# Kernel optimization log

Hardware: AMD Instinct MI355X
Metric: run time of the kernel (lower is better)

Reference implementation:

```python
import jax, jax.numpy as jnp
import numpy as np

N, E, G = 50000, 500000, 64
DIN, ED, H1, H2, HD, OUT = 128, 32, 256, 128, 64, 8


def setup_inputs() -> dict:
    key = jax.random.key(0)
    ks = jax.random.split(key, 20)
    g = lambda i, shape: (jax.random.normal(ks[i], shape, jnp.float32) * 0.05)
    return dict(
        node_attr=jax.random.normal(ks[0], (N, DIN), jnp.float32),
        edge_attr=jax.random.normal(ks[1], (E, ED), jnp.float32),
        edge_src=jax.random.randint(ks[2], (E,), 0, N, jnp.int32),
        edge_dst=jax.random.randint(ks[3], (E,), 0, N, jnp.int32),
        batch=jnp.sort(jax.random.randint(ks[4], (N,), 0, G, jnp.int32)),
        Wl1=g(5, (DIN, H1)), bl1=jnp.zeros((H1,), jnp.float32),
        Wr1=g(6, (DIN, H1)), br1=jnp.zeros((H1,), jnp.float32),
        We1=g(7, (ED, H1)), att1=g(8, (H1,)), b1=jnp.zeros((H1,), jnp.float32),
        Wl2=g(9, (H1, H2)), bl2=jnp.zeros((H2,), jnp.float32),
        Wr2=g(10, (H1, H2)), br2=jnp.zeros((H2,), jnp.float32),
        We2=g(11, (ED, H2)), att2=g(12, (H2,)), b2=jnp.zeros((H2,), jnp.float32),
        Wd1=g(13, (H2, HD)), bd1=jnp.zeros((HD,), jnp.float32),
        bn_gamma=jnp.ones((HD,), jnp.float32), bn_beta=jnp.zeros((HD,), jnp.float32),
        bn_mean=jnp.zeros((HD,), jnp.float32), bn_var=jnp.ones((HD,), jnp.float32),
        Wd2=g(14, (HD, OUT)), bd2=jnp.zeros((OUT,), jnp.float32),
    )


def gatv2(x, src, dst, eattr, Wl, bl, Wr, br, We, att, bias, n):
    # PyG GATv2Conv, heads=1: add self-loops (fill_value='mean' for edge_attr)
    ones = jnp.ones((eattr.shape[0],), x.dtype)
    deg = jax.ops.segment_sum(ones, dst, n)
    loop_attr = jax.ops.segment_sum(eattr, dst, n) / jnp.maximum(deg, 1.0)[:, None]
    loop = jnp.arange(n, dtype=src.dtype)
    src_ = jnp.concatenate([src, loop])
    dst_ = jnp.concatenate([dst, loop])
    eattr_ = jnp.concatenate([eattr, loop_attr], axis=0)
    xl = x @ Wl + bl  # [n, C] source transform (lin_l)
    xr = x @ Wr + br  # [n, C] dest transform (lin_r)
    # edge-wise GATv2 score: a^T LeakyReLU(xl_j + xr_i + We e_ij)
    e = jax.nn.leaky_relu(xl[src_] + xr[dst_] + eattr_ @ We, 0.2) @ att  # [E+n]
    m = jax.ops.segment_max(e, dst_, n)
    w = jnp.exp(e - m[dst_])
    denom = jax.ops.segment_sum(w, dst_, n)
    alpha = w / denom[dst_]
    return jax.ops.segment_sum(alpha[:, None] * xl[src_], dst_, n) + bias


def reference(node_attr, edge_attr, edge_src, edge_dst, batch,
              Wl1, bl1, Wr1, br1, We1, att1, b1,
              Wl2, bl2, Wr2, br2, We2, att2, b2,
              Wd1, bd1, bn_gamma, bn_beta, bn_mean, bn_var, Wd2, bd2):
    x = jax.nn.relu(gatv2(node_attr, edge_src, edge_dst, edge_attr,
                          Wl1, bl1, Wr1, br1, We1, att1, b1, N))
    x = jax.nn.relu(gatv2(x, edge_src, edge_dst, edge_attr,
                          Wl2, bl2, Wr2, br2, We2, att2, b2, N))
    # global mean pool over graphs
    cnt = jax.ops.segment_sum(jnp.ones((N,), x.dtype), batch, G)
    x = jax.ops.segment_sum(x, batch, G) / jnp.maximum(cnt, 1.0)[:, None]
    x = x @ Wd1 + bd1
    # BatchNorm1d in eval mode (running stats); dropout is identity in eval
    x = (x - bn_mean) / jnp.sqrt(bn_var + 1e-5) * bn_gamma + bn_beta
    x = jax.nn.leaky_relu(x, 0.1)
    return x @ Wd2 + bd2
```

## Files before the change

### kernel.cpp

```cpp
#include <hip/hip_runtime.h>
#include <cstdint>
#include <cstddef>
#include <cmath>

constexpr int Nn = 50000;
constexpr int Ne = 500000;
constexpr int Gg = 64;
constexpr int DIN = 128, ED = 32, H1 = 256, H2 = 128, HD = 64, NOUT = 8;

typedef __attribute__((ext_vector_type(8))) short bf16x8;
typedef __attribute__((ext_vector_type(4))) float f32x4;

__device__ __forceinline__ unsigned short f2bf(float x) {
    unsigned u = __float_as_uint(x);
    u += 0x7FFFu + ((u >> 16) & 1u);
    return (unsigned short)(u >> 16);
}
__device__ __forceinline__ float bf2f(unsigned short h) {
    return __uint_as_float(((unsigned)h) << 16);
}

__global__ void count_deg_kernel(const int* __restrict__ dst, int* __restrict__ deg) {
    int e = blockIdx.x * 256 + threadIdx.x;
    if (e < Ne) atomicAdd(&deg[dst[e]], 1);
}

__global__ __launch_bounds__(1024) void scan_kernel(const int* __restrict__ deg,
                                                    int* __restrict__ row_start) {
    __shared__ int part[1024];
    int t = threadIdx.x;
    const int chunk = (Nn + 1023) / 1024;
    int lo = t * chunk;
    int hi = min(lo + chunk, Nn);
    int s = 0;
    for (int i = lo; i < hi; i++) s += deg[i];
    part[t] = s;
    __syncthreads();
    for (int off = 1; off < 1024; off <<= 1) {
        int add = (t >= off) ? part[t - off] : 0;
        __syncthreads();
        part[t] += add;
        __syncthreads();
    }
    int base = (t == 0) ? 0 : part[t - 1];
    for (int i = lo; i < hi; i++) { row_start[i] = base; base += deg[i]; }
    if (t == 0) row_start[Nn] = Ne;
}

__global__ void scatter_kernel(const int* __restrict__ dst, const int* __restrict__ row_start,
                               int* __restrict__ cursor, int* __restrict__ perm) {
    int e = blockIdx.x * 256 + threadIdx.x;
    if (e < Ne) {
        int d = dst[e];
        int p = atomicAdd(&cursor[d], 1);
        perm[row_start[d] + p] = e;
    }
}

__global__ void build_sd_kernel(const int* __restrict__ perm, const int* __restrict__ src,
                                const int* __restrict__ dst,
                                int* __restrict__ srcv, int* __restrict__ dstv) {
    int j = blockIdx.x * 256 + threadIdx.x;
    if (j < Ne) {
        int e = perm[j];
        srcv[j] = src[e];
        dstv[j] = dst[e];
    }
}

__global__ void loop_attr_kernel(const int* __restrict__ row_start, const int* __restrict__ perm,
                                 const float* __restrict__ eattr, float* __restrict__ loop_attr) {
    int tid = blockIdx.x * 256 + threadIdx.x;
    if (tid >= Nn * 8) return;
    int i = tid >> 3, q = (tid & 7) << 2;
    int r0 = row_start[i], r1 = row_start[i + 1];
    float4 s = make_float4(0.f, 0.f, 0.f, 0.f);
    for (int j = r0; j < r1; j++) {
        int e = perm[j];
        float4 v = *(const float4*)(eattr + (size_t)e * ED + q);
        s.x += v.x; s.y += v.y; s.z += v.z; s.w += v.w;
    }
    float inv = 1.0f / fmaxf((float)(r1 - r0), 1.0f);
    *(float4*)(loop_attr + (size_t)i * ED + q) =
        make_float4(s.x * inv, s.y * inv, s.z * inv, s.w * inv);
}

__global__ void cvt_split_kernel(const float* __restrict__ src,
                                 unsigned short* __restrict__ hi,
                                 unsigned short* __restrict__ lo, int n4) {
    int idx = blockIdx.x * 256 + threadIdx.x;
    if (idx >= n4) return;
    float4 v = *(const float4*)(src + (size_t)idx * 4);
    float x[4] = {v.x, v.y, v.z, v.w};
    unsigned short h[4], l[4];
#pragma unroll
    for (int c = 0; c < 4; c++) {
        h[c] = f2bf(x[c]);
        l[c] = f2bf(x[c] - bf2f(h[c]));
    }
    *(ushort4*)(hi + (size_t)idx * 4) = make_ushort4(h[0], h[1], h[2], h[3]);
    *(ushort4*)(lo + (size_t)idx * 4) = make_ushort4(l[0], l[1], l[2], l[3]);
}

__global__ void cvt_W_kernel(const float* __restrict__ We,
                             unsigned short* __restrict__ whi,
                             unsigned short* __restrict__ wlo, int C) {
    int t = blockIdx.x * 256 + threadIdx.x;
    if (t >= C * ED) return;
    int c = t >> 5, k = t & 31;
    float x = We[(size_t)k * C + c];
    unsigned short h = f2bf(x);
    whi[t] = h;
    wlo[t] = f2bf(x - bf2f(h));
}

__global__ __launch_bounds__(256) void gemm_bias2_kernel(const float* __restrict__ A,
                                                         const float* __restrict__ W0,
                                                         const float* __restrict__ bias0,
                                                         float* __restrict__ C0,
                                                         const float* __restrict__ W1,
                                                         const float* __restrict__ bias1,
                                                         float* __restrict__ C1,
                                                         int M, int K, int Ncols) {
    const float* W = blockIdx.z ? W1 : W0;
    const float* bias = blockIdx.z ? bias1 : bias0;
    float* C = blockIdx.z ? C1 : C0;
    __shared__ float As[16][68];
    __shared__ float Bs[16][68];
    const int m0 = blockIdx.y * 64, n0 = blockIdx.x * 64;
    const int tid = threadIdx.x;
    const int tx = tid & 15, ty = tid >> 4;
    float acc[4][4] = {};
    const int ar = tid >> 2, ac4 = (tid & 3) << 2;
    const int br = tid >> 4, bc4 = (tid & 15) << 2;
    const bool arow_ok = (m0 + ar < M);

    float4 av = make_float4(0.f, 0.f, 0.f, 0.f);
    if (arow_ok) av = *(const float4*)(A + (size_t)(m0 + ar) * K + ac4);
    float4 bv = *(const float4*)(W + (size_t)br * Ncols + n0 + bc4);

    for (int k0 = 0; k0 < K; k0 += 16) {
        As[ac4 + 0][ar] = av.x; As[ac4 + 1][ar] = av.y;
        As[ac4 + 2][ar] = av.z; As[ac4 + 3][ar] = av.w;
        *(float4*)&Bs[br][bc4] = bv;
        __syncthreads();
        if (k0 + 16 < K) {
            if (arow_ok) av = *(const float4*)(A + (size_t)(m0 + ar) * K + k0 + 16 + ac4);
            bv = *(const float4*)(W + (size_t)(k0 + 16 + br) * Ncols + n0 + bc4);
        }
#pragma unroll
        for (int k = 0; k < 16; k++) {
            float a[4], b[4];
#pragma unroll
            for (int i = 0; i < 4; i++) a[i] = As[k][ty * 4 + i];
#pragma unroll
            for (int j = 0; j < 4; j++) b[j] = Bs[k][tx * 4 + j];
#pragma unroll
            for (int i = 0; i < 4; i++)
#pragma unroll
                for (int j = 0; j < 4; j++) acc[i][j] = fmaf(a[i], b[j], acc[i][j]);
        }
        __syncthreads();
    }
#pragma unroll
    for (int i = 0; i < 4; i++) {
        int m = m0 + ty * 4 + i;
        if (m < M) {
            float4 o;
            o.x = acc[i][0] + bias[n0 + tx * 4 + 0];
            o.y = acc[i][1] + bias[n0 + tx * 4 + 1];
            o.z = acc[i][2] + bias[n0 + tx * 4 + 2];
            o.w = acc[i][3] + bias[n0 + tx * 4 + 3];
            *(float4*)(C + (size_t)m * Ncols + n0 + tx * 4) = o;
        }
    }
}

template <int C>
__global__ __launch_bounds__((C / 64) * 64) void score_mfma3_kernel(
    int count, const int* __restrict__ perm,
    const int* __restrict__ srcv, const int* __restrict__ dstv,
    const unsigned short* __restrict__ ehi, const unsigned short* __restrict__ elo,
    const float* __restrict__ xl, const float* __restrict__ xr,
    const unsigned short* __restrict__ wthi, const unsigned short* __restrict__ wtlo,
    const float* __restrict__ att, float* __restrict__ sc_out) {
    constexpr int WPB = C / 64;
    constexpr int NTHR = WPB * 64;
    __shared__ unsigned short Ah[64 * 40], Al[64 * 40];
    __shared__ float pw[WPB][64];
    const int tid = threadIdx.x;
    const int j0 = blockIdx.x * 64;

    for (int t = tid; t < 64 * 4; t += NTHR) {
        int row = t >> 2, part = t & 3;
        int j = min(j0 + row, count - 1);
        int e = perm ? perm[j] : j;
        *(uint4*)&Ah[row * 40 + part * 8] = *(const uint4*)(ehi + (size_t)e * ED + part * 8);
        *(uint4*)&Al[row * 40 + part * 8] = *(const uint4*)(elo + (size_t)e * ED + part * 8);
    }
    __syncthreads();

    const int wv = tid >> 6, lane = tid & 63;
    const int g = lane >> 4, li = lane & 15;
    const int cb = wv * 64 + g * 4;

    bf16x8 af_h[4], af_l[4];
#pragma unroll
    for (int m = 0; m < 4; m++) {
        int col = wv * 64 + m * 16 + li;
        af_h[m] = *(const bf16x8*)(wthi + (size_t)col * ED + g * 8);
        af_l[m] = *(const bf16x8*)(wtlo + (size_t)col * ED + g * 8);
    }
    float4 attv[4];
#pragma unroll
    for (int m = 0; m < 4; m++) attv[m] = *(const float4*)(att + cb + m * 16);

    int s0, d0, s1, d1, s2, d2, s3, d3;
    {
        int j;
        j = min(j0 + 0 * 16 + li, count - 1); s0 = srcv ? srcv[j] : j; d0 = dstv ? dstv[j] : j;
        j = min(j0 + 1 * 16 + li, count - 1); s1 = srcv ? srcv[j] : j; d1 = dstv ? dstv[j] : j;
        j = min(j0 + 2 * 16 + li, count - 1); s2 = srcv ? srcv[j] : j; d2 = dstv ? dstv[j] : j;
        j = min(j0 + 3 * 16 + li, count - 1); s3 = srcv ? srcv[j] : j; d3 = dstv ? dstv[j] : j;
    }

    auto pf = [&](int n, int sE, int dE, bf16x8& bh, bf16x8& bl,
                  float4 (&xlv)[4], float4 (&xrv)[4]) {
        bh = *(const bf16x8*)&Ah[(n * 16 + li) * 40 + g * 8];
        bl = *(const bf16x8*)&Al[(n * 16 + li) * 40 + g * 8];
        const float* pl = xl + (size_t)sE * C + cb;
        const float* pr = xr + (size_t)dE * C + cb;
#pragma unroll
        for (int m = 0; m < 4; m++) {
            xlv[m] = *(const float4*)(pl + m * 16);
            xrv[m] = *(const float4*)(pr + m * 16);
        }
    };
    auto comp = [&](int n, bf16x8 bh, bf16x8 bl,
                    const float4 (&xlv)[4], const float4 (&xrv)[4]) {
        f32x4 acc[4];
#pragma unroll
        for (int m = 0; m < 4; m++) {
            acc[m][0] = xlv[m].x + xrv[m].x; acc[m][1] = xlv[m].y + xrv[m].y;
            acc[m][2] = xlv[m].z + xrv[m].z; acc[m][3] = xlv[m].w + xrv[m].w;
        }
#pragma unroll
        for (int m = 0; m < 4; m++) {
            acc[m] = __builtin_amdgcn_mfma_f32_16x16x32_bf16(af_h[m], bh, acc[m], 0, 0, 0);
            acc[m] = __builtin_amdgcn_mfma_f32_16x16x32_bf16(af_h[m], bl, acc[m], 0, 0, 0);
            acc[m] = __builtin_amdgcn_mfma_f32_16x16x32_bf16(af_l[m], bh, acc[m], 0, 0, 0);
        }
        float s = 0.f;
#pragma unroll
        for (int m = 0; m < 4; m++) {
            const float av[4] = {attv[m].x, attv[m].y, attv[m].z, attv[m].w};
#pragma unroll
            for (int r = 0; r < 4; r++) {
                float z = acc[m][r];
                z = z > 0.f ? z : 0.2f * z;
                s = fmaf(z, av[r], s);
            }
        }
        s += __shfl_xor(s, 16);
        s += __shfl_xor(s, 32);
        if (lane < 16) pw[wv][n * 16 + li] = s;
    };

    bf16x8 bhA, blA, bhB, blB;
    float4 xlA[4], xrA[4], xlB[4], xrB[4];
    pf(0, s0, d0, bhA, blA, xlA, xrA);
    pf(1, s1, d1, bhB, blB, xlB, xrB);
    comp(0, bhA, blA, xlA, xrA);
    pf(2, s2, d2, bhA, blA, xlA, xrA);
    comp(1, bhB, blB, xlB, xrB);
    pf(3, s3, d3, bhB, blB, xlB, xrB);
    comp(2, bhA, blA, xlA, xrA);
    comp(3, bhB, blB, xlB, xrB);

    __syncthreads();
    if (tid < 64) {
        float s = pw[0][tid];
#pragma unroll
        for (int w = 1; w < WPB; w++) s += pw[w][tid];
        int j = j0 + tid;
        if (j < count) sc_out[j] = s;
    }
}

template <int C>
__global__ __launch_bounds__(256) void aggregate2_kernel(
    const int* __restrict__ row_start, const int* __restrict__ srcv,
    const float* __restrict__ scores, const float* __restrict__ sscore,
    const float* __restrict__ xl, const float* __restrict__ bias,
    float* __restrict__ xout) {
    constexpr int VP = C / 64;
    const int wave = threadIdx.x >> 6, lane = threadIdx.x & 63;
    const int i = blockIdx.x * 4 + wave;
    if (i >= Nn) return;
    const int r0 = row_start[i], r1 = row_start[i + 1];

    float mx = sscore[i];
    for (int j = r0 + lane; j < r1; j += 64) mx = fmaxf(mx, scores[j]);
#pragma unroll
    for (int off = 32; off >= 1; off >>= 1) mx = fmaxf(mx, __shfl_xor(mx, off));

    float l = 0.f;
    float acc[VP];
#pragma unroll
    for (int j = 0; j < VP; j++) acc[j] = 0.f;

    float wA[4], xA[4][VP];
    auto load_batch = [&](int j0, float* w, float (*x)[VP]) {
#pragma unroll
        for (int q = 0; q < 4; q++) {
            int j = min(j0 + q, r1 - 1);
            w[q] = scores[j];
            const float* p = xl + (size_t)srcv[j] * C + lane * VP;
            if constexpr (VP == 4) {
                float4 v = *(const float4*)p;
                x[q][0] = v.x; x[q][1] = v.y; x[q][2] = v.z; x[q][3] = v.w;
            } else {
                float2 v = *(const float2*)p;
                x[q][0] = v.x; x[q][1] = v.y;
            }
        }
    };
    if (r0 < r1) load_batch(r0, wA, xA);

    for (int j0 = r0; j0 < r1; j0 += 4) {
        float wB[4], xB[4][VP];
        if (j0 + 4 < r1) load_batch(j0 + 4, wB, xB);
        const int nb = min(4, r1 - j0);
        for (int q = 0; q < nb; q++) {
            float w = __expf(wA[q] - mx);
            l += w;
#pragma unroll
            for (int j = 0; j < VP; j++) acc[j] = fmaf(w, xA[q][j], acc[j]);
        }
        if (j0 + 4 < r1) {
#pragma unroll
            for (int q = 0; q < 4; q++) {
                wA[q] = wB[q];
#pragma unroll
                for (int j = 0; j < VP; j++) xA[q][j] = xB[q][j];
            }
        }
    }

    {
        float w = __expf(sscore[i] - mx);
        l += w;
        const float* p = xl + (size_t)i * C + lane * VP;
        if constexpr (VP == 4) {
            float4 v = *(const float4*)p;
            acc[0] = fmaf(w, v.x, acc[0]); acc[1] = fmaf(w, v.y, acc[1]);
            acc[2] = fmaf(w, v.z, acc[2]); acc[3] = fmaf(w, v.w, acc[3]);
        } else {
            float2 v = *(const float2*)p;
            acc[0] = fmaf(w, v.x, acc[0]); acc[1] = fmaf(w, v.y, acc[1]);
        }
    }

    float invl = 1.0f / l;
    float* xo = xout + (size_t)i * C + lane * VP;
    if constexpr (VP == 4) {
        float4 bv = *(const float4*)(bias + lane * 4);
        float4 o;
        o.x = fmaxf(fmaf(acc[0], invl, bv.x), 0.f);
        o.y = fmaxf(fmaf(acc[1], invl, bv.y), 0.f);
        o.z = fmaxf(fmaf(acc[2], invl, bv.z), 0.f);
        o.w = fmaxf(fmaf(acc[3], invl, bv.w), 0.f);
        *(float4*)xo = o;
    } else {
        float2 bv = *(const float2*)(bias + lane * 2);
        float2 o;
        o.x = fmaxf(fmaf(acc[0], invl, bv.x), 0.f);
        o.y = fmaxf(fmaf(acc[1], invl, bv.y), 0.f);
        *(float2*)xo = o;
    }
}

__global__ __launch_bounds__(128) void pool2_kernel(const float* __restrict__ x2,
                                                    const int* __restrict__ batch,
                                                    float* __restrict__ pooled,
                                                    float* __restrict__ cnt) {
    const int c = threadIdx.x;
    const int chunk = (Nn + gridDim.x - 1) / gridDim.x;
    int lo = blockIdx.x * chunk;
    int hi = min(lo + chunk, Nn);
    if (lo >= hi) return;
    int gcur = batch[lo];
    float acc = 0.f, ncnt = 0.f;
    for (int i = lo; i < hi; i++) {
        int g = batch[i];
        if (g != gcur) {
            atomicAdd(&pooled[gcur * H2 + c], acc);
            if (c == 0) atomicAdd(&cnt[gcur], ncnt);
            acc = 0.f; ncnt = 0.f; gcur = g;
        }
        acc += x2[(size_t)i * H2 + c];
        ncnt += 1.f;
    }
    atomicAdd(&pooled[gcur * H2 + c], acc);
    if (c == 0) atomicAdd(&cnt[gcur], ncnt);
}

__global__ __launch_bounds__(64) void head_kernel(
    const float* __restrict__ pooled, const float* __restrict__ cnt,
    const float* __restrict__ Wd1, const float* __restrict__ bd1,
    const float* __restrict__ gamma, const float* __restrict__ beta,
    const float* __restrict__ mean, const float* __restrict__ var,
    const float* __restrict__ Wd2, const float* __restrict__ bd2,
    float* __restrict__ out) {
    __shared__ float xm[H2];
    __shared__ float h[HD];
    int g = blockIdx.x, t = threadIdx.x;
    float c = fmaxf(cnt[g], 1.0f);
    for (int i = t; i < H2; i += 64) xm[i] = pooled[g * H2 + i] / c;
    __syncthreads();
    float a = bd1[t];
    for (int k = 0; k < H2; k++) a = fmaf(xm[k], Wd1[k * HD + t], a);
    a = (a - mean[t]) / sqrtf(var[t] + 1e-5f) * gamma[t] + beta[t];
    a = a > 0.f ? a : 0.1f * a;
    h[t] = a;
    __syncthreads();
    if (t < NOUT) {
        float o = bd2[t];
        for (int k = 0; k < HD; k++) o = fmaf(h[k], Wd2[k * NOUT + t], o);
        out[g * NOUT + t] = o;
    }
}

extern "C" void kernel_launch(void* const* d_in, const int* in_sizes, int n_in,
                              void* d_out, int out_size, void* d_ws, size_t ws_size,
                              hipStream_t stream) {
    const float* node_attr = (const float*)d_in[0];
    const float* edge_attr = (const float*)d_in[1];
    const int* edge_src = (const int*)d_in[2];
    const int* edge_dst = (const int*)d_in[3];
    const int* batch = (const int*)d_in[4];
    const float* Wl1 = (const float*)d_in[5];  const float* bl1 = (const float*)d_in[6];
    const float* Wr1 = (const float*)d_in[7];  const float* br1 = (const float*)d_in[8];
    const float* We1 = (const float*)d_in[9];  const float* att1 = (const float*)d_in[10];
    const float* b1 = (const float*)d_in[11];
    const float* Wl2 = (const float*)d_in[12]; const float* bl2 = (const float*)d_in[13];
    const float* Wr2 = (const float*)d_in[14]; const float* br2 = (const float*)d_in[15];
    const float* We2 = (const float*)d_in[16]; const float* att2 = (const float*)d_in[17];
    const float* b2 = (const float*)d_in[18];
    const float* Wd1 = (const float*)d_in[19]; const float* bd1 = (const float*)d_in[20];
    const float* bn_gamma = (const float*)d_in[21]; const float* bn_beta = (const float*)d_in[22];
    const float* bn_mean = (const float*)d_in[23];  const float* bn_var = (const float*)d_in[24];
    const float* Wd2 = (const float*)d_in[25]; const float* bd2 = (const float*)d_in[26];
    float* out = (float*)d_out;

    char* ws = (char*)d_ws;
    size_t off = 0;
    auto alloc = [&](size_t bytes) -> char* {
        char* p = ws + off;
        off = (off + bytes + 255) & ~(size_t)255;
        return p;
    };
    int* deg         = (int*)alloc((size_t)Nn * 4);
    int* row_start   = (int*)alloc((size_t)(Nn + 1) * 4);
    int* cursor      = (int*)alloc((size_t)Nn * 4);
    int* perm        = (int*)alloc((size_t)Ne * 4);
    int* srcv        = (int*)alloc((size_t)Ne * 4);
    int* dstv        = (int*)alloc((size_t)Ne * 4);
    float* loop_attr = (float*)alloc((size_t)Nn * ED * 4);
    float* scores    = (float*)alloc((size_t)Ne * 4);
    float* sscore    = (float*)alloc((size_t)Nn * 4);
    float* pooled    = (float*)alloc((size_t)Gg * H2 * 4);
    float* cnt       = (float*)alloc((size_t)Gg * 4);
    float* xlb       = (float*)alloc((size_t)Nn * H1 * 4);
    float* xrb       = (float*)alloc((size_t)Nn * H1 * 4);
    float* x1        = (float*)alloc((size_t)Nn * H1 * 4);
    unsigned short* ehi = (unsigned short*)alloc((size_t)Ne * ED * 2);
    unsigned short* elo = (unsigned short*)alloc((size_t)Ne * ED * 2);
    unsigned short* lhi = (unsigned short*)alloc((size_t)Nn * ED * 2);
    unsigned short* llo = (unsigned short*)alloc((size_t)Nn * ED * 2);
    unsigned short* w1hi = (unsigned short*)alloc((size_t)H1 * ED * 2);
    unsigned short* w1lo = (unsigned short*)alloc((size_t)H1 * ED * 2);
    unsigned short* w2hi = (unsigned short*)alloc((size_t)H2 * ED * 2);
    unsigned short* w2lo = (unsigned short*)alloc((size_t)H2 * ED * 2);

    hipMemsetAsync(deg, 0, (size_t)Nn * 4, stream);
    hipMemsetAsync(cursor, 0, (size_t)Nn * 4, stream);
    hipMemsetAsync(pooled, 0, (size_t)Gg * H2 * 4, stream);
    hipMemsetAsync(cnt, 0, (size_t)Gg * 4, stream);

    count_deg_kernel<<<(Ne + 255) / 256, 256, 0, stream>>>(edge_dst, deg);
    scan_kernel<<<1, 1024, 0, stream>>>(deg, row_start);
    scatter_kernel<<<(Ne + 255) / 256, 256, 0, stream>>>(edge_dst, row_start, cursor, perm);
    build_sd_kernel<<<(Ne + 255) / 256, 256, 0, stream>>>(perm, edge_src, edge_dst, srcv, dstv);
    loop_attr_kernel<<<(Nn * 8 + 255) / 256, 256, 0, stream>>>(row_start, perm, edge_attr, loop_attr);

    cvt_split_kernel<<<(Ne * 8 + 255) / 256, 256, 0, stream>>>(edge_attr, ehi, elo, Ne * 8);
    cvt_split_kernel<<<(Nn * 8 + 255) / 256, 256, 0, stream>>>(loop_attr, lhi, llo, Nn * 8);
    cvt_W_kernel<<<(H1 * ED + 255) / 256, 256, 0, stream>>>(We1, w1hi, w1lo, H1);
    cvt_W_kernel<<<(H2 * ED + 255) / 256, 256, 0, stream>>>(We2, w2hi, w2lo, H2);

    const int eb64 = (Ne + 63) / 64, nb64 = (Nn + 63) / 64;

    gemm_bias2_kernel<<<dim3(H1 / 64, (Nn + 63) / 64, 2), 256, 0, stream>>>(
        node_attr, Wl1, bl1, xlb, Wr1, br1, xrb, Nn, DIN, H1);
    score_mfma3_kernel<H1><<<eb64, 256, 0, stream>>>(
        Ne, perm, srcv, dstv, ehi, elo, xlb, xrb, w1hi, w1lo, att1, scores);
    score_mfma3_kernel<H1><<<nb64, 256, 0, stream>>>(
        Nn, nullptr, nullptr, nullptr, lhi, llo, xlb, xrb, w1hi, w1lo, att1, sscore);
    aggregate2_kernel<H1><<<(Nn + 3) / 4, 256, 0, stream>>>(
        row_start, srcv, scores, sscore, xlb, b1, x1);

    gemm_bias2_kernel<<<dim3(H2 / 64, (Nn + 63) / 64, 2), 256, 0, stream>>>(
        x1, Wl2, bl2, xlb, Wr2, br2, xrb, Nn, H1, H2);
    score_mfma3_kernel<H2><<<eb64, 128, 0, stream>>>(
        Ne, perm, srcv, dstv, ehi, elo, xlb, xrb, w2hi, w2lo, att2, scores);
    score_mfma3_kernel<H2><<<nb64, 128, 0, stream>>>(
        Nn, nullptr, nullptr, nullptr, lhi, llo, xlb, xrb, w2hi, w2lo, att2, sscore);
    float* x2 = x1;
    aggregate2_kernel<H2><<<(Nn + 3) / 4, 256, 0, stream>>>(
        row_start, srcv, scores, sscore, xlb, b2, x2);

    pool2_kernel<<<256, 128, 0, stream>>>(x2, batch, pooled, cnt);
    head_kernel<<<Gg, 64, 0, stream>>>(pooled, cnt, Wd1, bd1, bn_gamma, bn_beta,
                                       bn_mean, bn_var, Wd2, bd2, out);
}
```

Measured before the change: 919.8 us.

## Replace FP32 SIMT node GEMMs with split-bf16 MFMA GEMMs

Swaps the scalar-FMA tiled GEMM for the lin_l/lin_r node transforms for an MFMA kernel. It emulates fp32 with hi/lo bf16 splits using three MFMAs per tile. Weights are pre-transposed and split by a generalized conversion kernel, and activations are split on the fly into shared memory. The aim is to cut GEMM compute time, at the cost of slightly reduced precision and weight fragments read straight from global memory without LDS staging.

```diff
diff --git a/kernel.cpp b/kernel.cpp
--- a/kernel.cpp
+++ b/kernel.cpp
@@ -102,78 +102,101 @@
     *(ushort4*)(lo + (size_t)idx * 4) = make_ushort4(l[0], l[1], l[2], l[3]);
 }
 
-__global__ void cvt_W_kernel(const float* __restrict__ We,
-                             unsigned short* __restrict__ whi,
-                             unsigned short* __restrict__ wlo, int C) {
+__global__ void cvt_wt_kernel(const float* __restrict__ W,
+                              unsigned short* __restrict__ hi,
+                              unsigned short* __restrict__ lo, int K, int N) {
     int t = blockIdx.x * 256 + threadIdx.x;
-    if (t >= C * ED) return;
-    int c = t >> 5, k = t & 31;
-    float x = We[(size_t)k * C + c];
+    if (t >= K * N) return;
+    int col = t / K, k = t % K;
+    float x = W[(size_t)k * N + col];
     unsigned short h = f2bf(x);
-    whi[t] = h;
-    wlo[t] = f2bf(x - bf2f(h));
-}
-
-__global__ __launch_bounds__(256) void gemm_bias2_kernel(const float* __restrict__ A,
-                                                         const float* __restrict__ W0,
-                                                         const float* __restrict__ bias0,
-                                                         float* __restrict__ C0,
-                                                         const float* __restrict__ W1,
-                                                         const float* __restrict__ bias1,
-                                                         float* __restrict__ C1,
-                                                         int M, int K, int Ncols) {
-    const float* W = blockIdx.z ? W1 : W0;
+    hi[t] = h;
+    lo[t] = f2bf(x - bf2f(h));
+}
+
+template <int K, int N>
+__global__ __launch_bounds__(256) void gemm_mfma_kernel(
+    int M, const float* __restrict__ A,
+    const unsigned short* __restrict__ wt0hi, const unsigned short* __restrict__ wt0lo,
+    const float* __restrict__ bias0, float* __restrict__ C0,
+    const unsigned short* __restrict__ wt1hi, const unsigned short* __restrict__ wt1lo,
+    const float* __restrict__ bias1, float* __restrict__ C1) {
+    const unsigned short* wthi = blockIdx.z ? wt1hi : wt0hi;
+    const unsigned short* wtlo = blockIdx.z ? wt1lo : wt0lo;
     const float* bias = blockIdx.z ? bias1 : bias0;
-    float* C = blockIdx.z ? C1 : C0;
-    __shared__ float As[16][68];
-    __shared__ float Bs[16][68];
-    const int m0 = blockIdx.y * 64, n0 = blockIdx.x * 64;
+    float* Cc = blockIdx.z ? C1 : C0;
+    constexpr int KC = (K > 128) ? 128 : K;
+    constexpr int P = KC + 8;
+    constexpr int NT = N / 64;
+    constexpr int CH = KC / 4;
+    __shared__ unsigned short Ah[64 * P], Al[64 * P];
     const int tid = threadIdx.x;
-    const int tx = tid & 15, ty = tid >> 4;
-    float acc[4][4] = {};
-    const int ar = tid >> 2, ac4 = (tid & 3) << 2;
-    const int br = tid >> 4, bc4 = (tid & 15) << 2;
-    const bool arow_ok = (m0 + ar < M);
-
-    float4 av = make_float4(0.f, 0.f, 0.f, 0.f);
-    if (arow_ok) av = *(const float4*)(A + (size_t)(m0 + ar) * K + ac4);
-    float4 bv = *(const float4*)(W + (size_t)br * Ncols + n0 + bc4);
-
-    for (int k0 = 0; k0 < K; k0 += 16) {
-        As[ac4 + 0][ar] = av.x; As[ac4 + 1][ar] = av.y;
-        As[ac4 + 2][ar] = av.z; As[ac4 + 3][ar] = av.w;
-        *(float4*)&Bs[br][bc4] = bv;
+    const int m0 = blockIdx.y * 64;
+
+    const int wv = tid >> 6, lane = tid & 63;
+    const int g = lane >> 4, li = lane & 15;
+    const int nb = wv * (N / 4);
+
+    f32x4 acc[4][NT];
+#pragma unroll
+    for (int n = 0; n < NT; n++) {
+        float bc = bias[nb + n * 16 + li];
+#pragma unroll
+        for (int m = 0; m < 4; m++) {
+            acc[m][n][0] = bc; acc[m][n][1] = bc; acc[m][n][2] = bc; acc[m][n][3] = bc;
+        }
+    }
+
+    for (int kc = 0; kc < K; kc += KC) {
+        for (int t = tid; t < 64 * CH; t += 256) {
+            int row = t / CH, c = t % CH;
+            int gr = min(m0 + row, M - 1);
+            float4 v = *(const float4*)(A + (size_t)gr * K + kc + c * 4);
+            unsigned short h0 = f2bf(v.x), h1 = f2bf(v.y), h2 = f2bf(v.z), h3 = f2bf(v.w);
+            unsigned short l0 = f2bf(v.x - bf2f(h0)), l1 = f2bf(v.y - bf2f(h1));
+            unsigned short l2 = f2bf(v.z - bf2f(h2)), l3 = f2bf(v.w - bf2f(h3));
+            *(ushort4*)&Ah[row * P + c * 4] = make_ushort4(h0, h1, h2, h3);
+            *(ushort4*)&Al[row * P + c * 4] = make_ushort4(l0, l1, l2, l3);
+        }
         __syncthreads();
-        if (k0 + 16 < K) {
-            if (arow_ok) av = *(const float4*)(A + (size_t)(m0 + ar) * K + k0 + 16 + ac4);
-            bv = *(const float4*)(W + (size_t)(k0 + 16 + br) * Ncols + n0 + bc4);
-        }
-#pragma unroll
-        for (int k = 0; k < 16; k++) {
-            float a[4], b[4];
-#pragma unroll
-            for (int i = 0; i < 4; i++) a[i] = As[k][ty * 4 + i];
-#pragma unroll
-            for (int j = 0; j < 4; j++) b[j] = Bs[k][tx * 4 + j];
-#pragma unroll
-            for (int i = 0; i < 4; i++)
-#pragma unroll
-                for (int j = 0; j < 4; j++) acc[i][j] = fmaf(a[i], b[j], acc[i][j]);
+
+#pragma unroll
+        for (int kt = 0; kt < KC / 32; kt++) {
+            bf16x8 afh[4], afl[4], bfh[NT], bfl[NT];
+#pragma unroll
+            for (int m = 0; m < 4; m++) {
+                afh[m] = *(const bf16x8*)&Ah[(m * 16 + li) * P + kt * 32 + g * 8];
+                afl[m] = *(const bf16x8*)&Al[(m * 16 + li) * P + kt * 32 + g * 8];
+            }
+#pragma unroll
+            for (int n = 0; n < NT; n++) {
+                int col = nb + n * 16 + li;
+                bfh[n] = *(const bf16x8*)(wthi + (size_t)col * K + kc + kt * 32 + g * 8);
+                bfl[n] = *(const bf16x8*)(wtlo + (size_t)col * K + kc + kt * 32 + g * 8);
+            }
+#pragma unroll
+            for (int m = 0; m < 4; m++)
+#pragma unroll
+                for (int n = 0; n < NT; n++) {
+                    acc[m][n] = __builtin_amdgcn_mfma_f32_16x16x32_bf16(afh[m], bfh[n], acc[m][n], 0, 0, 0);
+                    acc[m][n] = __builtin_amdgcn_mfma_f32_16x16x32_bf16(afh[m], bfl[n], acc[m][n], 0, 0, 0);
+                    acc[m][n] = __builtin_amdgcn_mfma_f32_16x16x32_bf16(afl[m], bfh[n], acc[m][n], 0, 0, 0);
+                }
         }
         __syncthreads();
     }
-#pragma unroll
-    for (int i = 0; i < 4; i++) {
-        int m = m0 + ty * 4 + i;
-        if (m < M) {
-            float4 o;
-            o.x = acc[i][0] + bias[n0 + tx * 4 + 0];
-            o.y = acc[i][1] + bias[n0 + tx * 4 + 1];
-            o.z = acc[i][2] + bias[n0 + tx * 4 + 2];
-            o.w = acc[i][3] + bias[n0 + tx * 4 + 3];
-            *(float4*)(C + (size_t)m * Ncols + n0 + tx * 4) = o;
-        }
-    }
+
+#pragma unroll
+    for (int m = 0; m < 4; m++)
+#pragma unroll
+        for (int n = 0; n < NT; n++) {
+            int col = nb + n * 16 + li;
+#pragma unroll
+            for (int r = 0; r < 4; r++) {
+                int node = m0 + m * 16 + g * 4 + r;
+                if (node < M) Cc[(size_t)node * N + col] = acc[m][n][r];
+            }
+        }
 }
 
 template <int C>
@@ -482,6 +505,14 @@
     unsigned short* w1lo = (unsigned short*)alloc((size_t)H1 * ED * 2);
     unsigned short* w2hi = (unsigned short*)alloc((size_t)H2 * ED * 2);
     unsigned short* w2lo = (unsigned short*)alloc((size_t)H2 * ED * 2);
+    unsigned short* wl1hi = (unsigned short*)alloc((size_t)H1 * DIN * 2);
+    unsigned short* wl1lo = (unsigned short*)alloc((size_t)H1 * DIN * 2);
+    unsigned short* wr1hi = (unsigned short*)alloc((size_t)H1 * DIN * 2);
+    unsigned short* wr1lo = (unsigned short*)alloc((size_t)H1 * DIN * 2);
+    unsigned short* wl2hi = (unsigned short*)alloc((size_t)H2 * H1 * 2);
+    unsigned short* wl2lo = (unsigned short*)alloc((size_t)H2 * H1 * 2);
+    unsigned short* wr2hi = (unsigned short*)alloc((size_t)H2 * H1 * 2);
+    unsigned short* wr2lo = (unsigned short*)alloc((size_t)H2 * H1 * 2);
 
     hipMemsetAsync(deg, 0, (size_t)Nn * 4, stream);
     hipMemsetAsync(cursor, 0, (size_t)Nn * 4, stream);
@@ -496,13 +527,18 @@
 
     cvt_split_kernel<<<(Ne * 8 + 255) / 256, 256, 0, stream>>>(edge_attr, ehi, elo, Ne * 8);
     cvt_split_kernel<<<(Nn * 8 + 255) / 256, 256, 0, stream>>>(loop_attr, lhi, llo, Nn * 8);
-    cvt_W_kernel<<<(H1 * ED + 255) / 256, 256, 0, stream>>>(We1, w1hi, w1lo, H1);
-    cvt_W_kernel<<<(H2 * ED + 255) / 256, 256, 0, stream>>>(We2, w2hi, w2lo, H2);
+    cvt_wt_kernel<<<(H1 * ED + 255) / 256, 256, 0, stream>>>(We1, w1hi, w1lo, ED, H1);
+    cvt_wt_kernel<<<(H2 * ED + 255) / 256, 256, 0, stream>>>(We2, w2hi, w2lo, ED, H2);
+    cvt_wt_kernel<<<(DIN * H1 + 255) / 256, 256, 0, stream>>>(Wl1, wl1hi, wl1lo, DIN, H1);
+    cvt_wt_kernel<<<(DIN * H1 + 255) / 256, 256, 0, stream>>>(Wr1, wr1hi, wr1lo, DIN, H1);
+    cvt_wt_kernel<<<(H1 * H2 + 255) / 256, 256, 0, stream>>>(Wl2, wl2hi, wl2lo, H1, H2);
+    cvt_wt_kernel<<<(H1 * H2 + 255) / 256, 256, 0, stream>>>(Wr2, wr2hi, wr2lo, H1, H2);
 
     const int eb64 = (Ne + 63) / 64, nb64 = (Nn + 63) / 64;
-
-    gemm_bias2_kernel<<<dim3(H1 / 64, (Nn + 63) / 64, 2), 256, 0, stream>>>(
-        node_attr, Wl1, bl1, xlb, Wr1, br1, xrb, Nn, DIN, H1);
+    const int gb = (Nn + 63) / 64;
+
+    gemm_mfma_kernel<DIN, H1><<<dim3(1, gb, 2), 256, 0, stream>>>(
+        Nn, node_attr, wl1hi, wl1lo, bl1, xlb, wr1hi, wr1lo, br1, xrb);
     score_mfma3_kernel<H1><<<eb64, 256, 0, stream>>>(
         Ne, perm, srcv, dstv, ehi, elo, xlb, xrb, w1hi, w1lo, att1, scores);
     score_mfma3_kernel<H1><<<nb64, 256, 0, stream>>>(
@@ -510,8 +546,8 @@
     aggregate2_kernel<H1><<<(Nn + 3) / 4, 256, 0, stream>>>(
         row_start, srcv, scores, sscore, xlb, b1, x1);
 
-    gemm_bias2_kernel<<<dim3(H2 / 64, (Nn + 63) / 64, 2), 256, 0, stream>>>(
-        x1, Wl2, bl2, xlb, Wr2, br2, xrb, Nn, H1, H2);
+    gemm_mfma_kernel<H1, H2><<<dim3(1, gb, 2), 256, 0, stream>>>(
+        Nn, x1, wl2hi, wl2lo, bl2, xlb, wr2hi, wr2lo, br2, xrb);
     score_mfma3_kernel<H2><<<eb64, 128, 0, stream>>>(
         Ne, perm, srcv, dstv, ehi, elo, xlb, xrb, w2hi, w2lo, att2, scores);
     score_mfma3_kernel<H2><<<nb64, 128, 0, stream>>>(
```

Result: faster. 844.9 us (-8.1%).
